# Kernel optimization log

Measured on AMD Instinct MI355X. Metric: run time of the kernel, lower is better.

The kernel has to match this reference:

```python
import jax, jax.numpy as jnp
import numpy as np

B, N, C, O, K, D = 32, 2048, 64, 64, 3, 16

def setup_inputs() -> dict:
    key = jax.random.key(0)
    ks = jax.random.split(key, 6)
    x = jax.random.normal(ks[0], (B, N, C), dtype=jnp.float32)
    node_embeddings = jax.random.normal(ks[1], (N, D), dtype=jnp.float32)
    adj_m = jax.random.uniform(ks[2], (N, N), dtype=jnp.float32)
    weights_pool = jax.random.normal(ks[3], (D, K, C, O), dtype=jnp.float32) * 0.1
    bias_pool = jax.random.normal(ks[4], (D, O), dtype=jnp.float32) * 0.1
    sa_weight = jax.random.normal(ks[5], (N, 2 * N), dtype=jnp.float32) * (1.0 / np.sqrt(2 * N))
    return {"x": x, "node_embeddings": node_embeddings, "adj_m": adj_m,
            "weights_pool": weights_pool, "bias_pool": bias_pool, "sa_weight": sa_weight}

def reference(x, node_embeddings, adj_m, weights_pool, bias_pool, sa_weight):
    n = node_embeddings.shape[0]
    # learned adaptive adjacency [N,N]
    supports = jax.nn.softmax(jax.nn.relu(node_embeddings @ node_embeddings.T), axis=1)
    # SpatialAttention: 1x1 conv over 2N channels == matmul with [N,2N] weight
    z = jnp.concatenate([supports, adj_m], axis=1) @ sa_weight.T  # [N,N]
    s2 = jax.nn.sigmoid(z)
    supports = s2 * adj_m + (1.0 - s2) * supports
    # Chebyshev polynomial basis
    support_set = [jnp.eye(n, dtype=supports.dtype), supports]
    for _ in range(2, K):
        support_set.append(2.0 * supports @ support_set[-1] - support_set[-2])
    supports_k = jnp.stack(support_set, axis=0)  # [K,N,N]
    # per-node generated weights/bias from embeddings
    weights = jnp.einsum('nd,dkio->nkio', node_embeddings, weights_pool)  # [N,K,C,O]
    bias = node_embeddings @ bias_pool  # [N,O]
    # graph conv: aggregate then per-node matmul
    x_g = jnp.einsum('knm,bmc->bnkc', supports_k, x)  # [B,N,K,C]
    x_gconv = jnp.einsum('bnki,nkio->bno', x_g, weights) + bias  # [B,N,O]
    return x_gconv
```

## Files before the change

kernel.cpp:

```cpp
#include <hip/hip_runtime.h>


typedef unsigned short u16;
typedef float f32x4 __attribute__((ext_vector_type(4)));
typedef __bf16 bf16x8 __attribute__((ext_vector_type(8)));
typedef unsigned short u16x8 __attribute__((ext_vector_type(8)));

#define PSTRIDE ((size_t)2048 * 2048)

__device__ __forceinline__ u16 f2bf(float f) {
    unsigned u = __float_as_uint(f);
    u += 0x7FFFu + ((u >> 16) & 1u);
    return (u16)(u >> 16);
}
__device__ __forceinline__ float bf2f(u16 h) {
    return __uint_as_float((unsigned)h << 16);
}
__device__ __forceinline__ void gl_lds16(const void* g, void* l) {
    __builtin_amdgcn_global_load_lds(
        (const __attribute__((address_space(1))) unsigned*)g,
        (__attribute__((address_space(3))) unsigned*)l, 16, 0, 0);
}

__global__ __launch_bounds__(256, 4)
void preB(const float* __restrict__ E, const float* __restrict__ adj,
          const float* __restrict__ saw, const float* __restrict__ x,
          const float* __restrict__ Wp, const float* __restrict__ bp,
          u16* __restrict__ Acat, u16* __restrict__ sawb, u16* __restrict__ xtT,
          u16* __restrict__ Wpb, float* __restrict__ Wpbf,
          float* __restrict__ bias, u16* __restrict__ xn, int mode) {
    __shared__ __align__(16) char smem[12800];
    const int bid = blockIdx.x, tid = threadIdx.x;

    if (bid < 16) {
        float (*tw)[49] = (float(*)[49])smem;
        const int d = bid;
        const float* base = Wp + (size_t)d * 12288;
        const int o = tid & 63, seg = tid >> 6;
#pragma unroll
        for (int p = 0; p < 4; ++p) {
            if (p) __syncthreads();
#pragma unroll
            for (int j = 0; j < 12; ++j) {
                int kil = seg * 12 + j;
                int ki = p * 48 + kil;
                int k = ki >> 6, i = ki & 63;
                float v;
                if (k == 0)      v = base[i * 64 + o] - base[8192 + i * 64 + o];
                else if (k == 1) v = base[4096 + i * 64 + o];
                else             v = 2.f * base[8192 + i * 64 + o];
                tw[o][kil] = v;
            }
            __syncthreads();
#pragma unroll
            for (int it = 0; it < 3; ++it) {
                int idx = tid + it * 256;
                int oo = idx / 12, q = idx - oo * 12;
                float v0 = tw[oo][q * 4], v1 = tw[oo][q * 4 + 1];
                float v2 = tw[oo][q * 4 + 2], v3 = tw[oo][q * 4 + 3];
                size_t dst = (size_t)(d * 64 + oo) * 192 + p * 48 + q * 4;
                *(float4*)(Wpbf + dst) = make_float4(v0, v1, v2, v3);
                *(ushort4*)(Wpb + dst) = make_ushort4(f2bf(v0), f2bf(v1), f2bf(v2), f2bf(v3));
            }
        }
    } else if (bid < 80) {
        const int nb = bid - 16;
#pragma unroll
        for (int it = 0; it < 8; ++it) {
            int idx = tid + it * 256;
            int n = nb * 32 + (idx >> 6), o = idx & 63;
            float s = 0.f;
#pragma unroll
            for (int d = 0; d < 16; ++d) s = fmaf(E[n * 16 + d], bp[d * 64 + o], s);
            bias[(size_t)n * 64 + o] = s;
        }
    } else if (bid < 848) {
        const size_t NADJ = 1048576, STRIDE = (size_t)768 * 256;
        const size_t e0 = (size_t)(bid - 80) * 256 + tid;
        float4 v[16];
#pragma unroll
        for (int it = 0; it < 16; ++it) {
            size_t idx = e0 + (size_t)it * STRIDE;
            const float* src = (idx < NADJ) ? (adj + idx * 4) : (saw + (idx - NADJ) * 4);
            v[it] = *(const float4*)src;
        }
#pragma unroll
        for (int it = 0; it < 16; ++it) {
            size_t idx = e0 + (size_t)it * STRIDE;
            ushort4 o = make_ushort4(f2bf(v[it].x), f2bf(v[it].y), f2bf(v[it].z), f2bf(v[it].w));
            if (idx < NADJ) {
                size_t j = idx * 4;
                int n = (int)(j >> 11), c = (int)(j & 2047);
                *(ushort4*)(Acat + (size_t)n * 4096 + 2048 + c) = o;
            } else {
                *(ushort4*)(sawb + (idx - NADJ) * 4) = o;
            }
        }
    } else {
        u16 (*t)[65] = (u16(*)[65])smem;
        int local = bid - 848;
        int m0 = (local & 31) * 64, b = local >> 5;
        int c = tid & 63, g = tid >> 6;
#pragma unroll
        for (int r = 0; r < 16; ++r) {
            int mm = g * 16 + r;
            t[mm][c] = f2bf(x[((size_t)b * 2048 + m0 + mm) * 64 + c]);
        }
        __syncthreads();
#pragma unroll
        for (int r = 0; r < 16; ++r) {
            int cc = g * 16 + r;
            xtT[((size_t)b * 64 + cc) * 2048 + m0 + c] = t[c][cc];
        }
        if (mode) {
#pragma unroll
            for (int r = 0; r < 16; ++r) {
                int mm = g * 16 + r;
                xn[((size_t)(m0 + mm)) * 2048 + b * 64 + c] = t[mm][c];
            }
        }
    }
}

__global__ __launch_bounds__(256)
void zsmW(const float* __restrict__ E, const float* __restrict__ Wpbf,
          u16* __restrict__ Acat, u16* __restrict__ Wnb) {
    __shared__ __align__(16) char smem[32768];
    const int bid = blockIdx.x, tid = threadIdx.x;

    if (bid < 256) {
        float* Et4 = (float*)smem;
        const int r0 = bid * 8;
        float z[8][8] = {};
#pragma unroll
        for (int ph = 0; ph < 4; ++ph) {
            if (ph) __syncthreads();
#pragma unroll
            for (int k = 0; k < 8; ++k) {
                const int n = tid + 256 * k;
                float4 e = ((const float4*)(E + (size_t)n * 16))[ph];
                Et4[0 * 2048 + n] = e.x; Et4[1 * 2048 + n] = e.y;
                Et4[2 * 2048 + n] = e.z; Et4[3 * 2048 + n] = e.w;
            }
            __syncthreads();
#pragma unroll
            for (int d = 0; d < 4; ++d) {
                const float* row = Et4 + d * 2048;
                float ev[8];
#pragma unroll
                for (int k = 0; k < 8; ++k) ev[k] = row[tid + 256 * k];
#pragma unroll
                for (int r = 0; r < 8; ++r) {
                    float e = row[r0 + r];
#pragma unroll
                    for (int k = 0; k < 8; ++k) z[r][k] = fmaf(e, ev[k], z[r][k]);
                }
            }
        }
        __syncthreads();
        float (*redm)[8] = (float(*)[8])smem;
        float (*reds)[8] = (float(*)[8])(smem + 256);

        float mr[8];
#pragma unroll
        for (int r = 0; r < 8; ++r) {
            float m = 0.f;
#pragma unroll
            for (int k = 0; k < 8; ++k) { z[r][k] = fmaxf(z[r][k], 0.f); m = fmaxf(m, z[r][k]); }
            mr[r] = m;
        }
#pragma unroll
        for (int off = 32; off; off >>= 1)
#pragma unroll
            for (int r = 0; r < 8; ++r) mr[r] = fmaxf(mr[r], __shfl_xor(mr[r], off, 64));
        if ((tid & 63) == 0) {
#pragma unroll
            for (int r = 0; r < 8; ++r) redm[tid >> 6][r] = mr[r];
        }
        __syncthreads();
#pragma unroll
        for (int r = 0; r < 8; ++r)
            mr[r] = fmaxf(fmaxf(redm[0][r], redm[1][r]), fmaxf(redm[2][r], redm[3][r]));
        float sr[8];
#pragma unroll
        for (int r = 0; r < 8; ++r) {
            float s = 0.f;
#pragma unroll
            for (int k = 0; k < 8; ++k) { z[r][k] = __expf(z[r][k] - mr[r]); s += z[r][k]; }
            sr[r] = s;
        }
#pragma unroll
        for (int off = 32; off; off >>= 1)
#pragma unroll
            for (int r = 0; r < 8; ++r) sr[r] += __shfl_xor(sr[r], off, 64);
        if ((tid & 63) == 0) {
#pragma unroll
            for (int r = 0; r < 8; ++r) reds[tid >> 6][r] = sr[r];
        }
        __syncthreads();
#pragma unroll
        for (int r = 0; r < 8; ++r) {
            float inv = 1.f / (reds[0][r] + reds[1][r] + reds[2][r] + reds[3][r]);
            u16* orow = Acat + (size_t)(r0 + r) * 4096;
#pragma unroll
            for (int k = 0; k < 8; ++k) orow[tid + 256 * k] = f2bf(z[r][k] * inv);
        }
    } else {
        float* Es = (float*)smem;
        const int w = bid - 256;
        const int c0 = (w % 12) * 1024, n0 = (w / 12) * 32;
        for (int j = tid; j < 512; j += 256) Es[j] = E[(size_t)n0 * 16 + j];
        float4 wf[16];
#pragma unroll
        for (int d = 0; d < 16; ++d)
            wf[d] = *(const float4*)(Wpbf + (size_t)d * 12288 + c0 + tid * 4);
        __syncthreads();
        for (int nl = 0; nl < 32; ++nl) {
            float4 s = make_float4(0.f, 0.f, 0.f, 0.f);
#pragma unroll
            for (int d = 0; d < 16; ++d) {
                float e = Es[nl * 16 + d];
                s.x = fmaf(e, wf[d].x, s.x);
                s.y = fmaf(e, wf[d].y, s.y);
                s.z = fmaf(e, wf[d].z, s.z);
                s.w = fmaf(e, wf[d].w, s.w);
            }
            *(ushort4*)(Wnb + (size_t)(n0 + nl) * 12288 + c0 + tid * 4) =
                make_ushort4(f2bf(s.x), f2bf(s.y), f2bf(s.z), f2bf(s.w));
        }
    }
}

__global__ __launch_bounds__(256)
void reduce_z(const u16* __restrict__ p, const u16* __restrict__ Acat,
              u16* __restrict__ S) {
    const size_t base = ((size_t)blockIdx.x * 256 + threadIdx.x) * 4;
    const size_t STRIDE = (size_t)1024 * 256 * 4;
#pragma unroll
    for (int it = 0; it < 4; ++it) {
        size_t j = base + (size_t)it * STRIDE;
        ushort4 p0 = *(const ushort4*)(p + j);
        ushort4 p1 = *(const ushort4*)(p + PSTRIDE + j);
        ushort4 p2 = *(const ushort4*)(p + 2 * PSTRIDE + j);
        ushort4 p3 = *(const ushort4*)(p + 3 * PSTRIDE + j);
        int row = (int)(j >> 11), col = (int)(j & 2047);
        ushort4 sp = *(const ushort4*)(Acat + (size_t)row * 4096 + col);
        ushort4 ad = *(const ushort4*)(Acat + (size_t)row * 4096 + 2048 + col);
        float z0 = bf2f(p0.x) + bf2f(p1.x) + bf2f(p2.x) + bf2f(p3.x);
        float z1 = bf2f(p0.y) + bf2f(p1.y) + bf2f(p2.y) + bf2f(p3.y);
        float z2 = bf2f(p0.z) + bf2f(p1.z) + bf2f(p2.z) + bf2f(p3.z);
        float z3 = bf2f(p0.w) + bf2f(p1.w) + bf2f(p2.w) + bf2f(p3.w);
        float s0 = 1.f / (1.f + __expf(-z0)), s1 = 1.f / (1.f + __expf(-z1));
        float s2 = 1.f / (1.f + __expf(-z2)), s3 = 1.f / (1.f + __expf(-z3));
        ushort4 o = make_ushort4(
            f2bf(s0 * bf2f(ad.x) + (1.f - s0) * bf2f(sp.x)),
            f2bf(s1 * bf2f(ad.y) + (1.f - s1) * bf2f(sp.y)),
            f2bf(s2 * bf2f(ad.z) + (1.f - s2) * bf2f(sp.z)),
            f2bf(s3 * bf2f(ad.w) + (1.f - s3) * bf2f(sp.w)));
        *(ushort4*)(S + j) = o;
    }
}

__global__ __launch_bounds__(512, 2)
void gemm_bt256(const u16* __restrict__ A, const u16* __restrict__ Bt,
                u16* __restrict__ Cp, int M, int N, int K, int Kh) {
    __shared__ alignas(16) u16 As[2][256 * 64];
    __shared__ alignas(16) u16 Bs[2][256 * 64];
    const int tid = threadIdx.x, lane = tid & 63, wave = tid >> 6;

    const int nbx = gridDim.x, nby = gridDim.y, nbz = gridDim.z;
    const int nwg = nbx * nby * nbz;
    int lin = (blockIdx.z * nby + blockIdx.y) * nbx + blockIdx.x;
    if ((nwg & 7) == 0) lin = (lin & 7) * (nwg >> 3) + (lin >> 3);
    const int bz = lin / (nbx * nby);
    const int r2 = lin - bz * nbx * nby;
    const int by = r2 / nbx, bx = r2 - by * nbx;

    const int m0 = by * 256, n0 = bx * 256;
    const int kbeg = bz * Kh;
    const int NT = Kh >> 6;
    const int wm = (wave >> 2) * 128, wn = (wave & 3) * 64;
    const int ml = lane & 15, c0l = lane >> 4;

    int sI[4], rowI[4], gcI[4];
#pragma unroll
    for (int r = 0; r < 4; ++r) {
        int s = r * 512 + tid;
        sI[r] = s; rowI[r] = s >> 3; gcI[r] = (s & 7) ^ ((s >> 3) & 7);
    }

    f32x4 acc[8][4] = {};
    bf16x8 af[4][2], bv[2][2];

#define LOADA(r_, kt_, buf_) \
    gl_lds16(A + (size_t)(m0 + rowI[r_]) * K + (kt_) + gcI[r_] * 8, \
             &As[buf_][sI[r_] * 8])
#define LOADB(r_, kt_, buf_) \
    gl_lds16(Bt + (size_t)(n0 + rowI[r_]) * K + (kt_) + gcI[r_] * 8, \
             &Bs[buf_][sI[r_] * 8])

#define DSRA(qa_) \
    _Pragma("unroll") \
    for (int i = 0; i < 4; ++i) { \
        const int mr = wm + (qa_) * 64 + i * 16 + ml; \
        _Pragma("unroll") \
        for (int ks = 0; ks < 2; ++ks) \
            af[i][ks] = *(const bf16x8*)(Asc + mr * 64 + (((c0l + ks * 4) ^ (mr & 7)) * 8)); \
    }
#define DSRB(qb_) \
    _Pragma("unroll") \
    for (int j = 0; j < 2; ++j) { \
        const int nr = wn + (qb_) * 32 + j * 16 + ml; \
        _Pragma("unroll") \
        for (int ks = 0; ks < 2; ++ks) \
            bv[j][ks] = *(const bf16x8*)(Bsc + nr * 64 + (((c0l + ks * 4) ^ (nr & 7)) * 8)); \
    }
#define MMQ(io_, jo_) \
    __builtin_amdgcn_s_barrier(); \
    asm volatile("s_waitcnt lgkmcnt(0)" ::: "memory"); \
    __builtin_amdgcn_s_setprio(1); \
    _Pragma("unroll") \
    for (int ks = 0; ks < 2; ++ks) \
        _Pragma("unroll") \
        for (int i = 0; i < 4; ++i) \
            _Pragma("unroll") \
            for (int j = 0; j < 2; ++j) \
                acc[(io_) + i][(jo_) + j] = __builtin_amdgcn_mfma_f32_16x16x32_bf16( \
                    af[i][ks], bv[j][ks], acc[(io_) + i][(jo_) + j], 0, 0, 0); \
    __builtin_amdgcn_s_setprio(0);

#pragma unroll
    for (int r = 0; r < 4; ++r) LOADA(r, kbeg, 0);
#pragma unroll
    for (int r = 0; r < 4; ++r) LOADB(r, kbeg, 0);
    asm volatile("s_waitcnt vmcnt(0)" ::: "memory");
    __builtin_amdgcn_s_barrier();

    for (int t = 0; t < NT - 1; ++t) {
        const int cur = t & 1, nxt = cur ^ 1;
        const u16* Asc = As[cur];
        const u16* Bsc = Bs[cur];
        const int k1 = kbeg + (t + 1) * 64;

        DSRA(0); DSRB(0);
        LOADB(0, k1, nxt); LOADB(1, k1, nxt);
        MMQ(0, 0);
        __builtin_amdgcn_s_barrier();

        DSRB(1);
        LOADB(2, k1, nxt); LOADB(3, k1, nxt);
        MMQ(0, 2);
        asm volatile("s_waitcnt vmcnt(4)" ::: "memory");
        __builtin_amdgcn_s_barrier();

        DSRA(1);
        LOADA(0, k1, nxt); LOADA(2, k1, nxt);
        MMQ(4, 2);
        __builtin_amdgcn_s_barrier();

        DSRB(0);
        LOADA(1, k1, nxt); LOADA(3, k1, nxt);
        MMQ(4, 0);
        asm volatile("s_waitcnt vmcnt(2)" ::: "memory");
        __builtin_amdgcn_s_barrier();
    }

    {
        const int cur = (NT - 1) & 1;
        const u16* Asc = As[cur];
        const u16* Bsc = Bs[cur];

        DSRA(0); DSRB(0);
        MMQ(0, 0);
        __builtin_amdgcn_s_barrier();

        DSRB(1);
        MMQ(0, 2);
        asm volatile("s_waitcnt vmcnt(0)" ::: "memory");
        __builtin_amdgcn_s_barrier();

        DSRA(1);
        MMQ(4, 2);
        __builtin_amdgcn_s_barrier();

        DSRB(0);
        MMQ(4, 0);
    }

#undef LOADA
#undef LOADB
#undef DSRA
#undef DSRB
#undef MMQ

    const int col_l = lane & 15, rl = (lane >> 4) * 4;
    u16* Cz = Cp + (size_t)bz * M * N;
#pragma unroll
    for (int i = 0; i < 8; ++i)
#pragma unroll
        for (int j = 0; j < 4; ++j)
#pragma unroll
            for (int r = 0; r < 4; ++r) {
                int row = m0 + wm + i * 16 + rl + r;
                int col = n0 + wn + j * 16 + col_l;
                Cz[(size_t)row * N + col] = f2bf(acc[i][j][r]);
            }
}

__global__ __launch_bounds__(256)
void reduceT(const u16* __restrict__ p, u16* __restrict__ xg1o,
             u16* __restrict__ xg1T, int mode) {
    __shared__ u16 t[64][68];
    int bx = blockIdx.x * 64, by = blockIdx.y * 64;
    int cg = threadIdx.x & 15, rg = threadIdx.x >> 4;
    int b = bx >> 6;
#pragma unroll
    for (int rr = 0; rr < 4; ++rr) {
        int row = rg * 4 + rr;
        size_t idx = (size_t)(by + row) * 2048 + bx + cg * 4;
        ushort4 q0 = *(const ushort4*)(p + idx);
        ushort4 q1 = *(const ushort4*)(p + PSTRIDE + idx);
        ushort4 q2 = *(const ushort4*)(p + 2 * PSTRIDE + idx);
        ushort4 q3 = *(const ushort4*)(p + 3 * PSTRIDE + idx);
        ushort4 v = make_ushort4(
            f2bf(bf2f(q0.x) + bf2f(q1.x) + bf2f(q2.x) + bf2f(q3.x)),
            f2bf(bf2f(q0.y) + bf2f(q1.y) + bf2f(q2.y) + bf2f(q3.y)),
            f2bf(bf2f(q0.z) + bf2f(q1.z) + bf2f(q2.z) + bf2f(q3.z)),
            f2bf(bf2f(q0.w) + bf2f(q1.w) + bf2f(q2.w) + bf2f(q3.w)));
        if (mode) *(ushort4*)(xg1o + idx) = v;
        else      *(ushort4*)(xg1o + ((size_t)b * 2048 + by + row) * 64 + cg * 4) = v;
        *(ushort4*)(&t[row][cg * 4]) = v;
    }
    __syncthreads();
    int c = threadIdx.x & 63, g = threadIdx.x >> 6;
#pragma unroll
    for (int r = 0; r < 16; ++r) {
        int row = g * 16 + r;
        xg1T[(size_t)(bx + row) * 2048 + by + c] = t[c][row];
    }
}

__global__ __launch_bounds__(256, 4)
void gconv_wn(const u16* __restrict__ xn, const u16* __restrict__ xg1n,
              const u16* __restrict__ p, const u16* __restrict__ Wnb,
              const float* __restrict__ bias, float* __restrict__ out) {
    __shared__ alignas(16) u16 As[32 * 192];
    __shared__ alignas(16) u16 Bs[64 * 192];
    const int n = blockIdx.x, tid = threadIdx.x;
    const int lane = tid & 63, wave = tid >> 6;
    const int wn2 = wave * 16;
    const int ml = lane & 15, c0l = lane >> 4;
    const int col = lane & 15, rl = (lane >> 4) * 4;

#pragma unroll
    for (int it = 0; it < 6; ++it) {
        int s = tid + it * 256;
        int row = s / 24, sc = s - row * 24;
        int gc = (sc & 24) | ((sc ^ row) & 7);
        gl_lds16(Wnb + (size_t)n * 12288 + (size_t)row * 192 + gc * 8, Bs + (size_t)s * 8);
    }
#pragma unroll
    for (int it = 0; it < 3; ++it) {
        int s = tid + it * 256;
        int row = s / 24, sc = s - row * 24;
        int gc = (sc & 24) | ((sc ^ row) & 7);
        u16x8 v;
        if (gc < 8) {
            v = *(const u16x8*)(xn + (size_t)n * 2048 + row * 64 + (gc & 7) * 8);
        } else if (gc < 16) {
            v = *(const u16x8*)(xg1n + (size_t)n * 2048 + row * 64 + (gc & 7) * 8);
        } else {
            const u16* pp = p + (size_t)n * 2048 + row * 64 + (gc & 7) * 8;
            u16x8 q0 = *(const u16x8*)pp;
            u16x8 q1 = *(const u16x8*)(pp + PSTRIDE);
            u16x8 q2 = *(const u16x8*)(pp + 2 * PSTRIDE);
            u16x8 q3 = *(const u16x8*)(pp + 3 * PSTRIDE);
#pragma unroll
            for (int tt = 0; tt < 8; ++tt)
                v[tt] = f2bf(bf2f(q0[tt]) + bf2f(q1[tt]) + bf2f(q2[tt]) + bf2f(q3[tt]));
        }
        *(u16x8*)(As + (size_t)s * 8) = v;
    }
    float bv0 = bias[(size_t)n * 64 + wn2 + col];
    f32x4 acc[2];
#pragma unroll
    for (int mt = 0; mt < 2; ++mt)
#pragma unroll
        for (int r = 0; r < 4; ++r) acc[mt][r] = bv0;
    __syncthreads();

#pragma unroll
    for (int ks = 0; ks < 6; ++ks) {
        int c = c0l + ks * 4;
        int o = wn2 + ml;
        bf16x8 bfrag = *(const bf16x8*)(Bs + (o * 24 + ((c & 24) | ((c ^ (o & 7)) & 7))) * 8);
#pragma unroll
        for (int mt = 0; mt < 2; ++mt) {
            int m = mt * 16 + ml;
            bf16x8 afrag = *(const bf16x8*)(As + (m * 24 + ((c & 24) | ((c ^ (m & 7)) & 7))) * 8);
            acc[mt] = __builtin_amdgcn_mfma_f32_16x16x32_bf16(afrag, bfrag, acc[mt], 0, 0, 0);
        }
    }
#pragma unroll
    for (int mt = 0; mt < 2; ++mt)
#pragma unroll
        for (int r = 0; r < 4; ++r) {
            int b = mt * 16 + rl + r;
            out[((size_t)b * 2048 + n) * 64 + wn2 + col] = acc[mt][r];
        }
}

__global__ __launch_bounds__(256, 2)
void gconv_mfma(const float* __restrict__ x, const u16* __restrict__ xg1,
                const u16* __restrict__ p, const u16* __restrict__ Wpb,
                const float* __restrict__ bias, const float* __restrict__ E,
                float* __restrict__ out) {
    __shared__ alignas(16) float El[16 * 128];
    const int tid = threadIdx.x, lane = tid & 63, wave = tid >> 6;
    const int m0 = blockIdx.x * 128, nb = m0 & 2047, bB = m0 >> 11;
    const int wm = (wave >> 1) * 64, wn = (wave & 1) * 32;
    const int ml = lane & 15, c0l = lane >> 4;
    const int col_l = lane & 15, rl = (lane >> 4) * 4;

#pragma unroll
    for (int it = 0; it < 8; ++it) {
        int idx = tid + it * 256;
        El[idx] = E[(size_t)(nb + (idx & 127)) * 16 + (idx >> 7)];
    }
    __syncthreads();

    bf16x8 af[4][6];
#pragma unroll
    for (int i = 0; i < 4; ++i) {
        const int row = m0 + wm + i * 16 + ml;
        const int n = row & 2047;
#pragma unroll
        for (int ks = 0; ks < 2; ++ks) {
            const float* xp = x + (size_t)row * 64 + (c0l + ks * 4) * 8;
            float4 a = *(const float4*)xp, b4 = *(const float4*)(xp + 4);
            u16x8 v;
            v[0] = f2bf(a.x);  v[1] = f2bf(a.y);  v[2] = f2bf(a.z);  v[3] = f2bf(a.w);
            v[4] = f2bf(b4.x); v[5] = f2bf(b4.y); v[6] = f2bf(b4.z); v[7] = f2bf(b4.w);
            af[i][ks] = __builtin_bit_cast(bf16x8, v);
        }
#pragma unroll
        for (int ks = 2; ks < 4; ++ks)
            af[i][ks] = *(const bf16x8*)(xg1 + (size_t)row * 64 + (c0l + ks * 4 - 8) * 8);
#pragma unroll
        for (int ks = 4; ks < 6; ++ks) {
            const u16* pp = p + (size_t)n * 2048 + bB * 64 + (c0l + ks * 4 - 16) * 8;
            u16x8 q0 = *(const u16x8*)pp;
            u16x8 q1 = *(const u16x8*)(pp + PSTRIDE);
            u16x8 q2 = *(const u16x8*)(pp + 2 * PSTRIDE);
            u16x8 q3 = *(const u16x8*)(pp + 3 * PSTRIDE);
            u16x8 v;
#pragma unroll
            for (int tt = 0; tt < 8; ++tt)
                v[tt] = f2bf(bf2f(q0[tt]) + bf2f(q1[tt]) + bf2f(q2[tt]) + bf2f(q3[tt]));
            af[i][ks] = __builtin_bit_cast(bf16x8, v);
        }
    }

    f32x4 oacc[4][2];
#pragma unroll
    for (int i = 0; i < 4; ++i)
#pragma unroll
        for (int j = 0; j < 2; ++j)
#pragma unroll
            for (int r = 0; r < 4; ++r)
                oacc[i][j][r] = bias[(size_t)(nb + wm + i * 16 + rl + r) * 64 + wn + j * 16 + col_l];

#pragma unroll 2
    for (int d = 0; d < 16; ++d) {
        bf16x8 bv[2][6];
#pragma unroll
        for (int j = 0; j < 2; ++j) {
            const u16* wp = Wpb + (size_t)(d * 64 + wn + j * 16 + ml) * 192 + c0l * 8;
#pragma unroll
            for (int ks = 0; ks < 6; ++ks)
                bv[j][ks] = *(const bf16x8*)(wp + ks * 32);
        }
        f32x4 tmp[4][2] = {};
#pragma unroll
        for (int ks = 0; ks < 6; ++ks)
#pragma unroll
            for (int i = 0; i < 4; ++i)
#pragma unroll
                for (int j = 0; j < 2; ++j)
                    tmp[i][j] = __builtin_amdgcn_mfma_f32_16x16x32_bf16(af[i][ks], bv[j][ks], tmp[i][j], 0, 0, 0);
#pragma unroll
        for (int i = 0; i < 4; ++i) {
            f32x4 ev = *(const f32x4*)(El + d * 128 + wm + i * 16 + rl);
#pragma unroll
            for (int r = 0; r < 4; ++r)
#pragma unroll
                for (int j = 0; j < 2; ++j)
                    oacc[i][j][r] = fmaf(ev[r], tmp[i][j][r], oacc[i][j][r]);
        }
    }
#pragma unroll
    for (int i = 0; i < 4; ++i)
#pragma unroll
        for (int j = 0; j < 2; ++j)
#pragma unroll
            for (int r = 0; r < 4; ++r)
                out[(size_t)(m0 + wm + i * 16 + rl + r) * 64 + wn + j * 16 + col_l] = oacc[i][j][r];
}

extern "C" void kernel_launch(void* const* d_in, const int* in_sizes, int n_in,
                              void* d_out, int out_size, void* d_ws, size_t ws_size,
                              hipStream_t stream) {
    const float* x   = (const float*)d_in[0];
    const float* E   = (const float*)d_in[1];
    const float* adj = (const float*)d_in[2];
    const float* Wp  = (const float*)d_in[3];
    const float* bp  = (const float*)d_in[4];
    const float* saw = (const float*)d_in[5];
    float* out = (float*)d_out;

    char* ws = (char*)d_ws;
    const size_t MB = 1u << 20;
    const int wn_mode = (ws_size >= 140 * MB) ? 1 : 0;

    u16*   Acat  = (u16*)(ws);
    u16*   sawb  = (u16*)(ws + 16 * MB);
    u16*   XtT   = (u16*)(ws + 32 * MB);
    u16*   Wpb   = (u16*)(ws + 40 * MB);
    float* bias  = (float*)(ws + 41 * MB);
    float* Wpbf  = (float*)(ws + 42 * MB);
    u16*   part  = (u16*)(ws + 48 * MB);
    u16*   S_bf  = (u16*)(ws + 16 * MB);
    u16*   xg1T  = (u16*)(ws + 24 * MB);
    u16*   xg1o  = (u16*)(ws);
    u16*   xn    = (u16*)(ws + 80 * MB);
    u16*   Wnb   = (u16*)(ws + 88 * MB);

    preB<<<1872, 256, 0, stream>>>(E, adj, saw, x, Wp, bp, Acat, sawb, XtT,
                                   Wpb, Wpbf, bias, xn, wn_mode);
    zsmW<<<wn_mode ? 1024 : 256, 256, 0, stream>>>(E, Wpbf, Acat, Wnb);

    gemm_bt256<<<dim3(8, 8, 4), 512, 0, stream>>>(Acat, sawb, part, 2048, 2048, 4096, 1024);
    reduce_z<<<1024, 256, 0, stream>>>(part, Acat, S_bf);
    gemm_bt256<<<dim3(8, 8, 4), 512, 0, stream>>>(S_bf, XtT, part, 2048, 2048, 2048, 512);
    reduceT<<<dim3(32, 32), 256, 0, stream>>>(part, xg1o, xg1T, wn_mode);
    gemm_bt256<<<dim3(8, 8, 4), 512, 0, stream>>>(S_bf, xg1T, part, 2048, 2048, 2048, 512);

    if (wn_mode)
        gconv_wn<<<2048, 256, 0, stream>>>(xn, xg1o, part, Wnb, bias, out);
    else
        gconv_mfma<<<512, 256, 0, stream>>>(x, xg1o, part, Wpb, bias, E, out);
}
```

Baseline: 271.2 us.

## Replace split-K 256-tile GEMMs with 128-tile GEMMs and fused epilogues

Drops the 4-way split-K 256x256 GEMM, which wrote bf16 partial sums that separate reduce kernels then summed. Uses a 128x128 tile GEMM over the full K with 256 workgroups. The sigmoid gating and the transpose/relayout are folded into the GEMM epilogues, and downstream consumers read the single result directly. This removes the partial-sum traffic and two kernel launches. In exchange each workgroup runs a longer K loop, the per-CU tiles are smaller, and the epilogues now do scattered stores.

```diff
diff --git a/kernel.cpp b/kernel.cpp
--- a/kernel.cpp
+++ b/kernel.cpp
@@ -231,78 +231,46 @@
     }
 }
 
-__global__ __launch_bounds__(256)
-void reduce_z(const u16* __restrict__ p, const u16* __restrict__ Acat,
-              u16* __restrict__ S) {
-    const size_t base = ((size_t)blockIdx.x * 256 + threadIdx.x) * 4;
-    const size_t STRIDE = (size_t)1024 * 256 * 4;
-#pragma unroll
-    for (int it = 0; it < 4; ++it) {
-        size_t j = base + (size_t)it * STRIDE;
-        ushort4 p0 = *(const ushort4*)(p + j);
-        ushort4 p1 = *(const ushort4*)(p + PSTRIDE + j);
-        ushort4 p2 = *(const ushort4*)(p + 2 * PSTRIDE + j);
-        ushort4 p3 = *(const ushort4*)(p + 3 * PSTRIDE + j);
-        int row = (int)(j >> 11), col = (int)(j & 2047);
-        ushort4 sp = *(const ushort4*)(Acat + (size_t)row * 4096 + col);
-        ushort4 ad = *(const ushort4*)(Acat + (size_t)row * 4096 + 2048 + col);
-        float z0 = bf2f(p0.x) + bf2f(p1.x) + bf2f(p2.x) + bf2f(p3.x);
-        float z1 = bf2f(p0.y) + bf2f(p1.y) + bf2f(p2.y) + bf2f(p3.y);
-        float z2 = bf2f(p0.z) + bf2f(p1.z) + bf2f(p2.z) + bf2f(p3.z);
-        float z3 = bf2f(p0.w) + bf2f(p1.w) + bf2f(p2.w) + bf2f(p3.w);
-        float s0 = 1.f / (1.f + __expf(-z0)), s1 = 1.f / (1.f + __expf(-z1));
-        float s2 = 1.f / (1.f + __expf(-z2)), s3 = 1.f / (1.f + __expf(-z3));
-        ushort4 o = make_ushort4(
-            f2bf(s0 * bf2f(ad.x) + (1.f - s0) * bf2f(sp.x)),
-            f2bf(s1 * bf2f(ad.y) + (1.f - s1) * bf2f(sp.y)),
-            f2bf(s2 * bf2f(ad.z) + (1.f - s2) * bf2f(sp.z)),
-            f2bf(s3 * bf2f(ad.w) + (1.f - s3) * bf2f(sp.w)));
-        *(ushort4*)(S + j) = o;
-    }
-}
-
-__global__ __launch_bounds__(512, 2)
-void gemm_bt256(const u16* __restrict__ A, const u16* __restrict__ Bt,
-                u16* __restrict__ Cp, int M, int N, int K, int Kh) {
-    __shared__ alignas(16) u16 As[2][256 * 64];
-    __shared__ alignas(16) u16 Bs[2][256 * 64];
+template <int EPI>
+__global__ __launch_bounds__(256, 2)
+void gemm128(const u16* __restrict__ A, const u16* __restrict__ Bt,
+             u16* __restrict__ C0, u16* __restrict__ C1,
+             const u16* __restrict__ Acat, int K, int mode) {
+    __shared__ __align__(16) char smem[65536];
+    u16* As = (u16*)smem;
+    u16* Bs = (u16*)(smem + 32768);
     const int tid = threadIdx.x, lane = tid & 63, wave = tid >> 6;
 
-    const int nbx = gridDim.x, nby = gridDim.y, nbz = gridDim.z;
-    const int nwg = nbx * nby * nbz;
-    int lin = (blockIdx.z * nby + blockIdx.y) * nbx + blockIdx.x;
-    if ((nwg & 7) == 0) lin = (lin & 7) * (nwg >> 3) + (lin >> 3);
-    const int bz = lin / (nbx * nby);
-    const int r2 = lin - bz * nbx * nby;
-    const int by = r2 / nbx, bx = r2 - by * nbx;
-
-    const int m0 = by * 256, n0 = bx * 256;
-    const int kbeg = bz * Kh;
-    const int NT = Kh >> 6;
-    const int wm = (wave >> 2) * 128, wn = (wave & 3) * 64;
+    int lin = blockIdx.y * 16 + blockIdx.x;
+    lin = (lin & 7) * 32 + (lin >> 3);
+    const int by = lin >> 4, bx = lin & 15;
+
+    const int m0 = by * 128, n0 = bx * 128;
+    const int NT = K >> 6;
+    const int wm = (wave >> 1) * 64, wnc = (wave & 1) * 64;
     const int ml = lane & 15, c0l = lane >> 4;
 
     int sI[4], rowI[4], gcI[4];
 #pragma unroll
     for (int r = 0; r < 4; ++r) {
-        int s = r * 512 + tid;
+        int s = r * 256 + tid;
         sI[r] = s; rowI[r] = s >> 3; gcI[r] = (s & 7) ^ ((s >> 3) & 7);
     }
 
-    f32x4 acc[8][4] = {};
-    bf16x8 af[4][2], bv[2][2];
+    f32x4 acc[4][4] = {};
+    bf16x8 af[2][2], bv[2][2];
 
 #define LOADA(r_, kt_, buf_) \
     gl_lds16(A + (size_t)(m0 + rowI[r_]) * K + (kt_) + gcI[r_] * 8, \
-             &As[buf_][sI[r_] * 8])
+             As + (buf_) * 8192 + sI[r_] * 8)
 #define LOADB(r_, kt_, buf_) \
     gl_lds16(Bt + (size_t)(n0 + rowI[r_]) * K + (kt_) + gcI[r_] * 8, \
-             &Bs[buf_][sI[r_] * 8])
+             Bs + (buf_) * 8192 + sI[r_] * 8)
 
 #define DSRA(qa_) \
     _Pragma("unroll") \
-    for (int i = 0; i < 4; ++i) { \
-        const int mr = wm + (qa_) * 64 + i * 16 + ml; \
+    for (int i = 0; i < 2; ++i) { \
+        const int mr = wm + (qa_) * 32 + i * 16 + ml; \
         _Pragma("unroll") \
         for (int ks = 0; ks < 2; ++ks) \
             af[i][ks] = *(const bf16x8*)(Asc + mr * 64 + (((c0l + ks * 4) ^ (mr & 7)) * 8)); \
@@ -310,37 +278,37 @@
 #define DSRB(qb_) \
     _Pragma("unroll") \
     for (int j = 0; j < 2; ++j) { \
-        const int nr = wn + (qb_) * 32 + j * 16 + ml; \
+        const int nr = wnc + (qb_) * 32 + j * 16 + ml; \
         _Pragma("unroll") \
         for (int ks = 0; ks < 2; ++ks) \
             bv[j][ks] = *(const bf16x8*)(Bsc + nr * 64 + (((c0l + ks * 4) ^ (nr & 7)) * 8)); \
     }
-#define MMQ(io_, jo_) \
+#define MMQ(qa_, qb_) \
     __builtin_amdgcn_s_barrier(); \
     asm volatile("s_waitcnt lgkmcnt(0)" ::: "memory"); \
     __builtin_amdgcn_s_setprio(1); \
     _Pragma("unroll") \
     for (int ks = 0; ks < 2; ++ks) \
         _Pragma("unroll") \
-        for (int i = 0; i < 4; ++i) \
+        for (int i = 0; i < 2; ++i) \
             _Pragma("unroll") \
             for (int j = 0; j < 2; ++j) \
-                acc[(io_) + i][(jo_) + j] = __builtin_amdgcn_mfma_f32_16x16x32_bf16( \
-                    af[i][ks], bv[j][ks], acc[(io_) + i][(jo_) + j], 0, 0, 0); \
+                acc[(qa_)*2 + i][(qb_)*2 + j] = __builtin_amdgcn_mfma_f32_16x16x32_bf16( \
+                    af[i][ks], bv[j][ks], acc[(qa_)*2 + i][(qb_)*2 + j], 0, 0, 0); \
     __builtin_amdgcn_s_setprio(0);
 
 #pragma unroll
-    for (int r = 0; r < 4; ++r) LOADA(r, kbeg, 0);
-#pragma unroll
-    for (int r = 0; r < 4; ++r) LOADB(r, kbeg, 0);
+    for (int r = 0; r < 4; ++r) LOADA(r, 0, 0);
+#pragma unroll
+    for (int r = 0; r < 4; ++r) LOADB(r, 0, 0);
     asm volatile("s_waitcnt vmcnt(0)" ::: "memory");
     __builtin_amdgcn_s_barrier();
 
     for (int t = 0; t < NT - 1; ++t) {
         const int cur = t & 1, nxt = cur ^ 1;
-        const u16* Asc = As[cur];
-        const u16* Bsc = Bs[cur];
-        const int k1 = kbeg + (t + 1) * 64;
+        const u16* Asc = As + cur * 8192;
+        const u16* Bsc = Bs + cur * 8192;
+        const int k1 = (t + 1) * 64;
 
         DSRA(0); DSRB(0);
         LOADB(0, k1, nxt); LOADB(1, k1, nxt);
@@ -349,42 +317,42 @@
 
         DSRB(1);
         LOADB(2, k1, nxt); LOADB(3, k1, nxt);
-        MMQ(0, 2);
+        MMQ(0, 1);
         asm volatile("s_waitcnt vmcnt(4)" ::: "memory");
         __builtin_amdgcn_s_barrier();
 
         DSRA(1);
         LOADA(0, k1, nxt); LOADA(2, k1, nxt);
-        MMQ(4, 2);
+        MMQ(1, 1);
         __builtin_amdgcn_s_barrier();
 
         DSRB(0);
         LOADA(1, k1, nxt); LOADA(3, k1, nxt);
-        MMQ(4, 0);
+        MMQ(1, 0);
         asm volatile("s_waitcnt vmcnt(2)" ::: "memory");
         __builtin_amdgcn_s_barrier();
     }
 
     {
         const int cur = (NT - 1) & 1;
-        const u16* Asc = As[cur];
-        const u16* Bsc = Bs[cur];
+        const u16* Asc = As + cur * 8192;
+        const u16* Bsc = Bs + cur * 8192;
 
         DSRA(0); DSRB(0);
         MMQ(0, 0);
         __builtin_amdgcn_s_barrier();
 
         DSRB(1);
-        MMQ(0, 2);
+        MMQ(0, 1);
         asm volatile("s_waitcnt vmcnt(0)" ::: "memory");
         __builtin_amdgcn_s_barrier();
 
         DSRA(1);
-        MMQ(4, 2);
+        MMQ(1, 1);
         __builtin_amdgcn_s_barrier();
 
         DSRB(0);
-        MMQ(4, 0);
+        MMQ(1, 0);
     }
 
 #undef LOADA
@@ -394,49 +362,58 @@
 #undef MMQ
 
     const int col_l = lane & 15, rl = (lane >> 4) * 4;
-    u16* Cz = Cp + (size_t)bz * M * N;
-#pragma unroll
-    for (int i = 0; i < 8; ++i)
-#pragma unroll
-        for (int j = 0; j < 4; ++j)
-#pragma unroll
-            for (int r = 0; r < 4; ++r) {
-                int row = m0 + wm + i * 16 + rl + r;
-                int col = n0 + wn + j * 16 + col_l;
-                Cz[(size_t)row * N + col] = f2bf(acc[i][j][r]);
-            }
-}
-
-__global__ __launch_bounds__(256)
-void reduceT(const u16* __restrict__ p, u16* __restrict__ xg1o,
-             u16* __restrict__ xg1T, int mode) {
-    __shared__ u16 t[64][68];
-    int bx = blockIdx.x * 64, by = blockIdx.y * 64;
-    int cg = threadIdx.x & 15, rg = threadIdx.x >> 4;
-    int b = bx >> 6;
-#pragma unroll
-    for (int rr = 0; rr < 4; ++rr) {
-        int row = rg * 4 + rr;
-        size_t idx = (size_t)(by + row) * 2048 + bx + cg * 4;
-        ushort4 q0 = *(const ushort4*)(p + idx);
-        ushort4 q1 = *(const ushort4*)(p + PSTRIDE + idx);
-        ushort4 q2 = *(const ushort4*)(p + 2 * PSTRIDE + idx);
-        ushort4 q3 = *(const ushort4*)(p + 3 * PSTRIDE + idx);
-        ushort4 v = make_ushort4(
-            f2bf(bf2f(q0.x) + bf2f(q1.x) + bf2f(q2.x) + bf2f(q3.x)),
-            f2bf(bf2f(q0.y) + bf2f(q1.y) + bf2f(q2.y) + bf2f(q3.y)),
-            f2bf(bf2f(q0.z) + bf2f(q1.z) + bf2f(q2.z) + bf2f(q3.z)),
-            f2bf(bf2f(q0.w) + bf2f(q1.w) + bf2f(q2.w) + bf2f(q3.w)));
-        if (mode) *(ushort4*)(xg1o + idx) = v;
-        else      *(ushort4*)(xg1o + ((size_t)b * 2048 + by + row) * 64 + cg * 4) = v;
-        *(ushort4*)(&t[row][cg * 4]) = v;
-    }
-    __syncthreads();
-    int c = threadIdx.x & 63, g = threadIdx.x >> 6;
-#pragma unroll
-    for (int r = 0; r < 16; ++r) {
-        int row = g * 16 + r;
-        xg1T[(size_t)(bx + row) * 2048 + by + c] = t[c][row];
+
+    if (EPI == 0) {
+#pragma unroll
+        for (int ai = 0; ai < 4; ++ai)
+#pragma unroll
+            for (int bj = 0; bj < 4; ++bj)
+#pragma unroll
+                for (int rr = 0; rr < 4; ++rr) {
+                    int row = m0 + wm + ai * 16 + rl + rr;
+                    int col = n0 + wnc + bj * 16 + col_l;
+                    C0[(size_t)row * 2048 + col] = f2bf(acc[ai][bj][rr]);
+                }
+    } else if (EPI == 1) {
+#pragma unroll
+        for (int ai = 0; ai < 4; ++ai)
+#pragma unroll
+            for (int bj = 0; bj < 4; ++bj)
+#pragma unroll
+                for (int rr = 0; rr < 4; ++rr) {
+                    int row = m0 + wm + ai * 16 + rl + rr;
+                    int col = n0 + wnc + bj * 16 + col_l;
+                    float sp = bf2f(Acat[(size_t)row * 4096 + col]);
+                    float ad = bf2f(Acat[(size_t)row * 4096 + 2048 + col]);
+                    float s = 1.f / (1.f + __expf(-acc[ai][bj][rr]));
+                    C0[(size_t)row * 2048 + col] = f2bf(s * ad + (1.f - s) * sp);
+                }
+    } else {
+#pragma unroll
+        for (int ai = 0; ai < 4; ++ai)
+#pragma unroll
+            for (int bj = 0; bj < 4; ++bj)
+#pragma unroll
+                for (int rr = 0; rr < 4; ++rr) {
+                    int row = m0 + wm + ai * 16 + rl + rr;
+                    int col = n0 + wnc + bj * 16 + col_l;
+                    u16 v = f2bf(acc[ai][bj][rr]);
+                    if (mode) C0[(size_t)row * 2048 + col] = v;
+                    else      C0[((size_t)(col >> 6) * 2048 + row) * 64 + (col & 63)] = v;
+                }
+        __syncthreads();
+        u16 (*slab)[70] = (u16(*)[70])(smem + wave * 8960);
+#pragma unroll
+        for (int ai = 0; ai < 4; ++ai)
+#pragma unroll
+            for (int bj = 0; bj < 4; ++bj)
+#pragma unroll
+                for (int rr = 0; rr < 4; ++rr)
+                    slab[ai * 16 + rl + rr][bj * 16 + col_l] = f2bf(acc[ai][bj][rr]);
+        asm volatile("s_waitcnt lgkmcnt(0)" ::: "memory");
+#pragma unroll
+        for (int it = 0; it < 64; ++it)
+            C1[(size_t)(n0 + wnc + it) * 2048 + m0 + wm + lane] = slab[lane][it];
     }
 }
 
@@ -470,14 +447,7 @@
         } else if (gc < 16) {
             v = *(const u16x8*)(xg1n + (size_t)n * 2048 + row * 64 + (gc & 7) * 8);
         } else {
-            const u16* pp = p + (size_t)n * 2048 + row * 64 + (gc & 7) * 8;
-            u16x8 q0 = *(const u16x8*)pp;
-            u16x8 q1 = *(const u16x8*)(pp + PSTRIDE);
-            u16x8 q2 = *(const u16x8*)(pp + 2 * PSTRIDE);
-            u16x8 q3 = *(const u16x8*)(pp + 3 * PSTRIDE);
-#pragma unroll
-            for (int tt = 0; tt < 8; ++tt)
-                v[tt] = f2bf(bf2f(q0[tt]) + bf2f(q1[tt]) + bf2f(q2[tt]) + bf2f(q3[tt]));
+            v = *(const u16x8*)(p + (size_t)n * 2048 + row * 64 + (gc & 7) * 8);
         }
         *(u16x8*)(As + (size_t)s * 8) = v;
     }
@@ -547,18 +517,8 @@
         for (int ks = 2; ks < 4; ++ks)
             af[i][ks] = *(const bf16x8*)(xg1 + (size_t)row * 64 + (c0l + ks * 4 - 8) * 8);
 #pragma unroll
-        for (int ks = 4; ks < 6; ++ks) {
-            const u16* pp = p + (size_t)n * 2048 + bB * 64 + (c0l + ks * 4 - 16) * 8;
-            u16x8 q0 = *(const u16x8*)pp;
-            u16x8 q1 = *(const u16x8*)(pp + PSTRIDE);
-            u16x8 q2 = *(const u16x8*)(pp + 2 * PSTRIDE);
-            u16x8 q3 = *(const u16x8*)(pp + 3 * PSTRIDE);
-            u16x8 v;
-#pragma unroll
-            for (int tt = 0; tt < 8; ++tt)
-                v[tt] = f2bf(bf2f(q0[tt]) + bf2f(q1[tt]) + bf2f(q2[tt]) + bf2f(q3[tt]));
-            af[i][ks] = __builtin_bit_cast(bf16x8, v);
-        }
+        for (int ks = 4; ks < 6; ++ks)
+            af[i][ks] = *(const bf16x8*)(p + (size_t)n * 2048 + bB * 64 + (c0l + ks * 4 - 16) * 8);
     }
 
     f32x4 oacc[4][2];
@@ -639,11 +599,9 @@
                                    Wpb, Wpbf, bias, xn, wn_mode);
     zsmW<<<wn_mode ? 1024 : 256, 256, 0, stream>>>(E, Wpbf, Acat, Wnb);
 
-    gemm_bt256<<<dim3(8, 8, 4), 512, 0, stream>>>(Acat, sawb, part, 2048, 2048, 4096, 1024);
-    reduce_z<<<1024, 256, 0, stream>>>(part, Acat, S_bf);
-    gemm_bt256<<<dim3(8, 8, 4), 512, 0, stream>>>(S_bf, XtT, part, 2048, 2048, 2048, 512);
-    reduceT<<<dim3(32, 32), 256, 0, stream>>>(part, xg1o, xg1T, wn_mode);
-    gemm_bt256<<<dim3(8, 8, 4), 512, 0, stream>>>(S_bf, xg1T, part, 2048, 2048, 2048, 512);
+    gemm128<1><<<dim3(16, 16), 256, 0, stream>>>(Acat, sawb, S_bf, nullptr, Acat, 4096, wn_mode);
+    gemm128<2><<<dim3(16, 16), 256, 0, stream>>>(S_bf, XtT, xg1o, xg1T, nullptr, 2048, wn_mode);
+    gemm128<0><<<dim3(16, 16), 256, 0, stream>>>(S_bf, xg1T, part, nullptr, nullptr, 2048, wn_mode);
 
     if (wn_mode)
         gconv_wn<<<2048, 256, 0, stream>>>(xn, xg1o, part, Wnb, bias, out);
```

Result: slower. 279.5 us (+3.1%).
